# Kernel optimization log

Hardware: AMD Instinct MI355X
Metric: run time of the kernel (lower is better)

Reference implementation:

```python
import jax, jax.numpy as jnp
import numpy as np
from jax import lax

WINDOW = 3  # box-filter window (matches init kwarg)


def setup_inputs() -> dict:
    key = jax.random.key(0)
    y_pred = jax.random.normal(key, (1, 3, 192, 192, 192), dtype=jnp.float32)
    return {"y_pred": y_pred}


def _box_filter(x, win):
    pad = win // 2
    kernel = jnp.ones((3, 1, win, win, win), dtype=x.dtype) / (win ** 3)
    return lax.conv_general_dilated(
        x, kernel,
        window_strides=(1, 1, 1),
        padding=[(pad, pad)] * 3,
        dimension_numbers=("NCDHW", "OIDHW", "NCDHW"),
        feature_group_count=3,
    )


def reference(y_pred):
    base = y_pred[:, :, :-1, :-1, :-1]
    dy = jnp.abs(y_pred[:, :, 1:, :-1, :-1] - base)
    dx = jnp.abs(y_pred[:, :, :-1, 1:, :-1] - base)
    dz = jnp.abs(y_pred[:, :, :-1, :-1, 1:] - base)

    fdx = _box_filter(dx, WINDOW)  # [B,3,D-1,H-1,W-1]
    fdy = _box_filter(dy, WINDOW)
    fdz = _box_filter(dz, WINDOW)

    dxdx, dxdy, dxdz = fdx[:, 1:2], fdy[:, 1:2], fdz[:, 1:2]
    dydx, dydy, dydz = fdx[:, 0:1], fdy[:, 0:1], fdz[:, 0:1]
    dzdx, dzdy, dzdz = fdx[:, 2:3], fdy[:, 2:3], fdz[:, 2:3]

    det_1 = (dxdx + 1) * ((dydy + 1) * (dzdz + 1) - dydz * dzdy)
    det_2 = -dxdy * (dydx * (dzdz + 1) - dydz * dzdx)
    det_3 = dxdz * (dydx * dzdy - (dydy + 1) * dzdx)
    J = det_1 + det_2 + det_3
    return jnp.squeeze(J)  # [D-1, H-1, W-1] for B=1
```

## Files before the change

kernel.cpp:

```cpp
#include <hip/hip_runtime.h>

#define NSZ   192
#define NSZ2  (NSZ*NSZ)
#define NSZ3  (NSZ*NSZ*NSZ)
#define N1    191
#define TW    64
#define TH    8
#define TD    8
#define LROWS 11
#define PADW  72
#define ROWF4 18
#define NROWS 33
#define SLOTF4 (NROWS*ROWF4)
#define SLOTF  (SLOTF4*4)
#define NTHREADS 256

__device__ __forceinline__ void ld3f2(float* d, const float* p) {
    *(float2*)&d[0] = *(const float2*)&p[0];
    *(float2*)&d[2] = *(const float2*)&p[2];
    *(float2*)&d[4] = *(const float2*)&p[4];
}

__global__ __launch_bounds__(NTHREADS)
void jac_kernel(const float* __restrict__ y, float* __restrict__ out) {
    __shared__ __align__(16) float lds[3 * SLOTF];

    const int tx = threadIdx.x;
    const int ty = threadIdx.y;
    const int tid = ty * 32 + tx;
    const int w0 = blockIdx.x * TW;
    const int h0 = blockIdx.y * TH;
    const int d0 = blockIdx.z * TD;
    const int j  = h0 + ty;
    const int k0 = w0 + 2 * tx;

    float mrow[3][4];
    #pragma unroll
    for (int r = 0; r < 3; ++r) {
        int gr = j - 1 + r;
        float rv = (gr >= 0 && gr < N1) ? 1.f : 0.f;
        #pragma unroll
        for (int p = 0; p < 4; ++p) {
            int gk = k0 - 1 + p;
            mrow[r][p] = (gk >= 0 && gk < N1) ? rv : 0.f;
        }
    }

    const bool has3 = (tid < SLOTF4 - 2 * NTHREADS);
    int goff[3];
    #pragma unroll
    for (int k = 0; k < 3; ++k) {
        int e4 = tid + k * NTHREADS;
        int e4c = e4 < SLOTF4 ? e4 : 0;
        int rowidx = e4c / ROWF4;
        int m   = e4c - rowidx * ROWF4;
        int ch  = rowidx / LROWS;
        int row = rowidx - ch * LROWS;
        int gr = h0 - 1 + row; gr = gr < 0 ? 0 : (gr > N1 ? N1 : gr);
        int c4 = w0 - 4 + 4 * m; c4 = c4 < 0 ? 0 : (c4 > NSZ - 4 ? NSZ - 4 : c4);
        goff[k] = ch * NSZ3 + gr * NSZ + c4;
    }

    float PS[18], T1[18];
    #pragma unroll
    for (int t = 0; t < 18; ++t) { PS[t] = 0.f; T1[t] = 0.f; }

    {
        float4 s0a, s0b, s0c, s1a, s1b, s1c;
        const bool p0 = (d0 >= 1);
        if (p0) {
            const float* b = y + (size_t)(d0 - 1) * NSZ2;
            s0a = *(const float4*)&b[goff[0]];
            s0b = *(const float4*)&b[goff[1]];
            if (has3) s0c = *(const float4*)&b[goff[2]];
        }
        {
            const float* b = y + (size_t)d0 * NSZ2;
            s1a = *(const float4*)&b[goff[0]];
            s1b = *(const float4*)&b[goff[1]];
            if (has3) s1c = *(const float4*)&b[goff[2]];
        }
        if (p0) {
            float* d = lds + ((d0 + 2) % 3) * SLOTF;
            *(float4*)&d[tid * 4] = s0a;
            *(float4*)&d[(tid + 256) * 4] = s0b;
            if (has3) *(float4*)&d[(tid + 512) * 4] = s0c;
        }
        {
            float* d = lds + (d0 % 3) * SLOTF;
            *(float4*)&d[tid * 4] = s1a;
            *(float4*)&d[(tid + 256) * 4] = s1b;
            if (has3) *(float4*)&d[(tid + 512) * 4] = s1c;
        }
    }
    __syncthreads();

    int sA = (d0 + 2) % 3;

    for (int ii = 0; ii < TD + 2; ++ii) {
        const int i  = d0 - 1 + ii;
        const int sB = sA == 2 ? 0 : sA + 1;
        const int sC = sB == 2 ? 0 : sB + 1;

        const bool doStage = (ii <= TD) && (i + 2 <= N1);
        float4 g0, g1, g2;
        if (doStage) {
            const float* b = y + (size_t)(i + 2) * NSZ2;
            g0 = *(const float4*)&b[goff[0]];
            g1 = *(const float4*)&b[goff[1]];
            if (has3) g2 = *(const float4*)&b[goff[2]];
        }

        float acc[18];
        #pragma unroll
        for (int t = 0; t < 18; ++t) acc[t] = 0.f;

        if (i >= 0 && i < N1) {
            #pragma unroll
            for (int c = 0; c < 3; ++c) {
                const float* pA = lds + sA * SLOTF + (c * LROWS + ty) * PADW + 2 * tx + 2;
                const float* pB = lds + sB * SLOTF + (c * LROWS + ty) * PADW + 2 * tx + 2;
                float Y0[6], Y1[6], Z0[6];
                ld3f2(Y0, pA);
                #pragma unroll
                for (int r = 0; r < 3; ++r) {
                    ld3f2(Y1, pA + (r + 1) * PADW);
                    ld3f2(Z0, pB + r * PADW);
                    float dxv[4], dyv[4], dzv[4];
                    #pragma unroll
                    for (int p = 0; p < 4; ++p) {
                        float m = mrow[r][p];
                        dxv[p] = fabsf(Y1[p + 1] - Y0[p + 1]) * m;
                        dyv[p] = fabsf(Z0[p + 1] - Y0[p + 1]) * m;
                        dzv[p] = fabsf(Y0[p + 2] - Y0[p + 1]) * m;
                    }
                    #pragma unroll
                    for (int q = 0; q < 2; ++q) {
                        acc[(c * 3 + 0) * 2 + q] += dxv[q] + dxv[q + 1] + dxv[q + 2];
                        acc[(c * 3 + 1) * 2 + q] += dyv[q] + dyv[q + 1] + dyv[q + 2];
                        acc[(c * 3 + 2) * 2 + q] += dzv[q] + dzv[q + 1] + dzv[q + 2];
                    }
                    #pragma unroll
                    for (int p = 0; p < 6; ++p) Y0[p] = Y1[p];
                }
            }
        }

        float f[18];
        #pragma unroll
        for (int t = 0; t < 18; ++t) {
            f[t]  = PS[t] + acc[t];
            PS[t] = T1[t] + acc[t];
            T1[t] = acc[t];
        }

        const int d = i - 1;
        if (ii >= 2 && d < N1 && j < N1) {
            const float s27 = 1.f / 27.f;
            #pragma unroll
            for (int q = 0; q < 2; ++q) {
                if (k0 + q < N1) {
                    float axx = f[(1*3+0)*2+q]*s27, axy = f[(1*3+1)*2+q]*s27, axz = f[(1*3+2)*2+q]*s27;
                    float ayx = f[(0*3+0)*2+q]*s27, ayy = f[(0*3+1)*2+q]*s27, ayz = f[(0*3+2)*2+q]*s27;
                    float azx = f[(2*3+0)*2+q]*s27, azy = f[(2*3+1)*2+q]*s27, azz = f[(2*3+2)*2+q]*s27;
                    float ee = ayy + 1.f, zz = azz + 1.f;
                    float J = (axx + 1.f) * (ee*zz - ayz*azy)
                            - axy * (ayx*zz - ayz*azx)
                            + axz * (ayx*azy - ee*azx);
                    out[(d * N1 + j) * N1 + (k0 + q)] = J;
                }
            }
        }

        if (doStage) {
            float* dst = lds + sC * SLOTF;
            *(float4*)&dst[tid * 4] = g0;
            *(float4*)&dst[(tid + 256) * 4] = g1;
            if (has3) *(float4*)&dst[(tid + 512) * 4] = g2;
        }
        __syncthreads();

        sA = sB;
    }
}

extern "C" void kernel_launch(void* const* d_in, const int* in_sizes, int n_in,
                              void* d_out, int out_size, void* d_ws, size_t ws_size,
                              hipStream_t stream) {
    const float* y = (const float*)d_in[0];
    float* out = (float*)d_out;
    dim3 grid(3, 24, 24);
    dim3 block(32, 8, 1);
    jac_kernel<<<grid, block, 0, stream>>>(y, out);
}
```

Baseline: 62.03 us.

## Stage input slices via direct global-to-LDS loads with taller tiles and 4 outputs/thread

Replaces register-staged global loads with __builtin_amdgcn_global_load_lds so slices go straight into LDS. The tile height doubles to 16, which cuts halo overhead, and each thread now computes 4 W-outputs instead of 2. The masking is split into separate column and row factors, and the 1/27 scaling is folded into a single final multiply. The goal is less register traffic and halo reload, at the cost of more registers (36-entry accumulators) and fewer blocks. The async LDS loads are ordered only by the existing __syncthreads, which relies on the compiler inserting a waitcnt.

```diff
diff --git a/kernel.cpp b/kernel.cpp
--- a/kernel.cpp
+++ b/kernel.cpp
@@ -5,55 +5,73 @@
 #define NSZ3  (NSZ*NSZ*NSZ)
 #define N1    191
 #define TW    64
-#define TH    8
+#define TH    16
 #define TD    8
-#define LROWS 11
+#define LROWS 19
 #define PADW  72
 #define ROWF4 18
-#define NROWS 33
-#define SLOTF4 (NROWS*ROWF4)
-#define SLOTF  (SLOTF4*4)
+#define SLOTF4R 1026
+#define SLOTF4P 1088
+#define SLOTF  (SLOTF4P*4)
 #define NTHREADS 256
 
-__device__ __forceinline__ void ld3f2(float* d, const float* p) {
+__device__ __forceinline__ void gload_lds16(const float* g, float* l) {
+    __builtin_amdgcn_global_load_lds((const __attribute__((address_space(1))) void*)g,
+                                     (__attribute__((address_space(3))) void*)l, 16, 0, 0);
+}
+
+__device__ __forceinline__ void ld8(float* d, const float* p) {
     *(float2*)&d[0] = *(const float2*)&p[0];
     *(float2*)&d[2] = *(const float2*)&p[2];
     *(float2*)&d[4] = *(const float2*)&p[4];
-}
-
-__global__ __launch_bounds__(NTHREADS)
+    *(float2*)&d[6] = *(const float2*)&p[6];
+}
+
+__device__ __forceinline__ void stage(const float* __restrict__ y, float* slot,
+                                      int s, const int* goff, int tid) {
+    const float* src = y + (size_t)s * NSZ2;
+    gload_lds16(src + goff[0], slot + (size_t)tid * 4);
+    gload_lds16(src + goff[1], slot + (size_t)(tid + 256) * 4);
+    gload_lds16(src + goff[2], slot + (size_t)(tid + 512) * 4);
+    gload_lds16(src + goff[3], slot + (size_t)(tid + 768) * 4);
+    if (tid < 64)
+        gload_lds16(src + goff[4], slot + (size_t)(1024 + tid) * 4);
+}
+
+#define IDX(c,dir,q) (((c)*3+(dir))*4+(q))
+
+__global__ __launch_bounds__(NTHREADS, 3)
 void jac_kernel(const float* __restrict__ y, float* __restrict__ out) {
     __shared__ __align__(16) float lds[3 * SLOTF];
 
     const int tx = threadIdx.x;
     const int ty = threadIdx.y;
-    const int tid = ty * 32 + tx;
+    const int tid = ty * 16 + tx;
     const int w0 = blockIdx.x * TW;
     const int h0 = blockIdx.y * TH;
     const int d0 = blockIdx.z * TD;
     const int j  = h0 + ty;
-    const int k0 = w0 + 2 * tx;
-
-    float mrow[3][4];
+    const int k0 = w0 + 4 * tx;
+
+    float colv[6], rowv[3];
+    #pragma unroll
+    for (int p = 0; p < 6; ++p) {
+        int gk = k0 - 1 + p;
+        colv[p] = (gk >= 0 && gk < N1) ? 1.f : 0.f;
+    }
     #pragma unroll
     for (int r = 0; r < 3; ++r) {
         int gr = j - 1 + r;
-        float rv = (gr >= 0 && gr < N1) ? 1.f : 0.f;
-        #pragma unroll
-        for (int p = 0; p < 4; ++p) {
-            int gk = k0 - 1 + p;
-            mrow[r][p] = (gk >= 0 && gk < N1) ? rv : 0.f;
-        }
-    }
-
-    const bool has3 = (tid < SLOTF4 - 2 * NTHREADS);
-    int goff[3];
-    #pragma unroll
-    for (int k = 0; k < 3; ++k) {
-        int e4 = tid + k * NTHREADS;
-        int e4c = e4 < SLOTF4 ? e4 : 0;
-        int rowidx = e4c / ROWF4;
-        int m   = e4c - rowidx * ROWF4;
+        rowv[r] = (gr >= 0 && gr < N1) ? 1.f : 0.f;
+    }
+
+    int goff[5];
+    #pragma unroll
+    for (int k = 0; k < 5; ++k) {
+        int e4 = (k < 4) ? (tid + k * 256) : (1024 + (tid & 63));
+        if (e4 > SLOTF4R - 1) e4 = SLOTF4R - 1;
+        int rowidx = e4 / ROWF4;
+        int m   = e4 - rowidx * ROWF4;
         int ch  = rowidx / LROWS;
         int row = rowidx - ch * LROWS;
         int gr = h0 - 1 + row; gr = gr < 0 ? 0 : (gr > N1 ? N1 : gr);
@@ -61,125 +79,114 @@
         goff[k] = ch * NSZ3 + gr * NSZ + c4;
     }
 
-    float PS[18], T1[18];
-    #pragma unroll
-    for (int t = 0; t < 18; ++t) { PS[t] = 0.f; T1[t] = 0.f; }
-
-    {
-        float4 s0a, s0b, s0c, s1a, s1b, s1c;
-        const bool p0 = (d0 >= 1);
-        if (p0) {
-            const float* b = y + (size_t)(d0 - 1) * NSZ2;
-            s0a = *(const float4*)&b[goff[0]];
-            s0b = *(const float4*)&b[goff[1]];
-            if (has3) s0c = *(const float4*)&b[goff[2]];
-        }
-        {
-            const float* b = y + (size_t)d0 * NSZ2;
-            s1a = *(const float4*)&b[goff[0]];
-            s1b = *(const float4*)&b[goff[1]];
-            if (has3) s1c = *(const float4*)&b[goff[2]];
-        }
-        if (p0) {
-            float* d = lds + ((d0 + 2) % 3) * SLOTF;
-            *(float4*)&d[tid * 4] = s0a;
-            *(float4*)&d[(tid + 256) * 4] = s0b;
-            if (has3) *(float4*)&d[(tid + 512) * 4] = s0c;
-        }
-        {
-            float* d = lds + (d0 % 3) * SLOTF;
-            *(float4*)&d[tid * 4] = s1a;
-            *(float4*)&d[(tid + 256) * 4] = s1b;
-            if (has3) *(float4*)&d[(tid + 512) * 4] = s1c;
-        }
-    }
+    float a1[36], a2[36];
+    #pragma unroll
+    for (int t = 0; t < 36; ++t) { a1[t] = 0.f; a2[t] = 0.f; }
+
+    if (d0 >= 1) stage(y, lds + ((d0 + 2) % 3) * SLOTF, d0 - 1, goff, tid);
+    stage(y, lds + (d0 % 3) * SLOTF, d0, goff, tid);
     __syncthreads();
 
     int sA = (d0 + 2) % 3;
+    const int wbase = 4 * tx + 2;
 
     for (int ii = 0; ii < TD + 2; ++ii) {
         const int i  = d0 - 1 + ii;
         const int sB = sA == 2 ? 0 : sA + 1;
         const int sC = sB == 2 ? 0 : sB + 1;
 
-        const bool doStage = (ii <= TD) && (i + 2 <= N1);
-        float4 g0, g1, g2;
-        if (doStage) {
-            const float* b = y + (size_t)(i + 2) * NSZ2;
-            g0 = *(const float4*)&b[goff[0]];
-            g1 = *(const float4*)&b[goff[1]];
-            if (has3) g2 = *(const float4*)&b[goff[2]];
-        }
-
-        float acc[18];
-        #pragma unroll
-        for (int t = 0; t < 18; ++t) acc[t] = 0.f;
+        if (ii <= TD && i + 2 <= N1)
+            stage(y, lds + sC * SLOTF, i + 2, goff, tid);
+
+        float f[36];
 
         if (i >= 0 && i < N1) {
             #pragma unroll
             for (int c = 0; c < 3; ++c) {
-                const float* pA = lds + sA * SLOTF + (c * LROWS + ty) * PADW + 2 * tx + 2;
-                const float* pB = lds + sB * SLOTF + (c * LROWS + ty) * PADW + 2 * tx + 2;
-                float Y0[6], Y1[6], Z0[6];
-                ld3f2(Y0, pA);
+                const float* pA = lds + sA * SLOTF + (c * LROWS + ty) * PADW + wbase;
+                const float* pB = lds + sB * SLOTF + (c * LROWS + ty) * PADW + wbase;
+                float acc[12];
+                float Y0[8], Y1[8], Z0[8];
+                ld8(Y0, pA);
                 #pragma unroll
                 for (int r = 0; r < 3; ++r) {
-                    ld3f2(Y1, pA + (r + 1) * PADW);
-                    ld3f2(Z0, pB + r * PADW);
-                    float dxv[4], dyv[4], dzv[4];
+                    ld8(Y1, pA + (r + 1) * PADW);
+                    ld8(Z0, pB + r * PADW);
+                    const float rv = rowv[r];
+                    float dH[6], dD[6], dW[6];
                     #pragma unroll
-                    for (int p = 0; p < 4; ++p) {
-                        float m = mrow[r][p];
-                        dxv[p] = fabsf(Y1[p + 1] - Y0[p + 1]) * m;
-                        dyv[p] = fabsf(Z0[p + 1] - Y0[p + 1]) * m;
-                        dzv[p] = fabsf(Y0[p + 2] - Y0[p + 1]) * m;
+                    for (int p = 0; p < 6; ++p) {
+                        const float cm = colv[p];
+                        dH[p] = fabsf(Y1[p + 1] - Y0[p + 1]) * cm;
+                        dD[p] = fabsf(Z0[p + 1] - Y0[p + 1]) * cm;
+                        dW[p] = fabsf(Y0[p + 2] - Y0[p + 1]) * cm;
+                    }
+                    {
+                        float e12 = dH[1] + dH[2], e34 = dH[3] + dH[4];
+                        float t0 = dH[0] + e12, t1 = e12 + dH[3];
+                        float t2 = dH[2] + e34, t3 = e34 + dH[5];
+                        if (r == 0) { acc[0] = rv * t0; acc[1] = rv * t1; acc[2] = rv * t2; acc[3] = rv * t3; }
+                        else { acc[0] = fmaf(rv, t0, acc[0]); acc[1] = fmaf(rv, t1, acc[1]);
+                               acc[2] = fmaf(rv, t2, acc[2]); acc[3] = fmaf(rv, t3, acc[3]); }
+                    }
+                    {
+                        float e12 = dD[1] + dD[2], e34 = dD[3] + dD[4];
+                        float t0 = dD[0] + e12, t1 = e12 + dD[3];
+                        float t2 = dD[2] + e34, t3 = e34 + dD[5];
+                        if (r == 0) { acc[4] = rv * t0; acc[5] = rv * t1; acc[6] = rv * t2; acc[7] = rv * t3; }
+                        else { acc[4] = fmaf(rv, t0, acc[4]); acc[5] = fmaf(rv, t1, acc[5]);
+                               acc[6] = fmaf(rv, t2, acc[6]); acc[7] = fmaf(rv, t3, acc[7]); }
+                    }
+                    {
+                        float e12 = dW[1] + dW[2], e34 = dW[3] + dW[4];
+                        float t0 = dW[0] + e12, t1 = e12 + dW[3];
+                        float t2 = dW[2] + e34, t3 = e34 + dW[5];
+                        if (r == 0) { acc[8] = rv * t0; acc[9] = rv * t1; acc[10] = rv * t2; acc[11] = rv * t3; }
+                        else { acc[8] = fmaf(rv, t0, acc[8]); acc[9] = fmaf(rv, t1, acc[9]);
+                               acc[10] = fmaf(rv, t2, acc[10]); acc[11] = fmaf(rv, t3, acc[11]); }
                     }
                     #pragma unroll
-                    for (int q = 0; q < 2; ++q) {
-                        acc[(c * 3 + 0) * 2 + q] += dxv[q] + dxv[q + 1] + dxv[q + 2];
-                        acc[(c * 3 + 1) * 2 + q] += dyv[q] + dyv[q + 1] + dyv[q + 2];
-                        acc[(c * 3 + 2) * 2 + q] += dzv[q] + dzv[q + 1] + dzv[q + 2];
-                    }
-                    #pragma unroll
-                    for (int p = 0; p < 6; ++p) Y0[p] = Y1[p];
+                    for (int p = 0; p < 8; ++p) Y0[p] = Y1[p];
+                }
+                #pragma unroll
+                for (int t = 0; t < 12; ++t) {
+                    const int gi = c * 12 + t;
+                    f[gi]  = a2[gi] + a1[gi] + acc[t];
+                    a2[gi] = a1[gi];
+                    a1[gi] = acc[t];
+                }
+            }
+        } else {
+            #pragma unroll
+            for (int t = 0; t < 36; ++t) {
+                f[t]  = a2[t] + a1[t];
+                a2[t] = a1[t];
+                a1[t] = 0.f;
+            }
+        }
+
+        const int d = i - 1;
+        if (ii >= 2 && d < N1 && j < N1) {
+            const float K = 27.f, KS = 1.f / 19683.f;
+            #pragma unroll
+            for (int q = 0; q < 4; ++q) {
+                if (k0 + q < N1) {
+                    float ayx = f[IDX(0,0,q)], ayy = f[IDX(0,1,q)], ayz = f[IDX(0,2,q)];
+                    float axx = f[IDX(1,0,q)], axy = f[IDX(1,1,q)], axz = f[IDX(1,2,q)];
+                    float azx = f[IDX(2,0,q)], azy = f[IDX(2,1,q)], azz = f[IDX(2,2,q)];
+                    float ayy27 = ayy + K, azz27 = azz + K, axx27 = axx + K;
+                    float t = fmaf(-ayz, azy, ayy27 * azz27);
+                    float v = fmaf(-ayz, azx, ayx * azz27);
+                    float w = fmaf(-ayy27, azx, ayx * azy);
+                    float R = axx27 * t;
+                    R = fmaf(-axy, v, R);
+                    R = fmaf(axz, w, R);
+                    out[(d * N1 + j) * N1 + (k0 + q)] = R * KS;
                 }
             }
         }
 
-        float f[18];
-        #pragma unroll
-        for (int t = 0; t < 18; ++t) {
-            f[t]  = PS[t] + acc[t];
-            PS[t] = T1[t] + acc[t];
-            T1[t] = acc[t];
-        }
-
-        const int d = i - 1;
-        if (ii >= 2 && d < N1 && j < N1) {
-            const float s27 = 1.f / 27.f;
-            #pragma unroll
-            for (int q = 0; q < 2; ++q) {
-                if (k0 + q < N1) {
-                    float axx = f[(1*3+0)*2+q]*s27, axy = f[(1*3+1)*2+q]*s27, axz = f[(1*3+2)*2+q]*s27;
-                    float ayx = f[(0*3+0)*2+q]*s27, ayy = f[(0*3+1)*2+q]*s27, ayz = f[(0*3+2)*2+q]*s27;
-                    float azx = f[(2*3+0)*2+q]*s27, azy = f[(2*3+1)*2+q]*s27, azz = f[(2*3+2)*2+q]*s27;
-                    float ee = ayy + 1.f, zz = azz + 1.f;
-                    float J = (axx + 1.f) * (ee*zz - ayz*azy)
-                            - axy * (ayx*zz - ayz*azx)
-                            + axz * (ayx*azy - ee*azx);
-                    out[(d * N1 + j) * N1 + (k0 + q)] = J;
-                }
-            }
-        }
-
-        if (doStage) {
-            float* dst = lds + sC * SLOTF;
-            *(float4*)&dst[tid * 4] = g0;
-            *(float4*)&dst[(tid + 256) * 4] = g1;
-            if (has3) *(float4*)&dst[(tid + 512) * 4] = g2;
-        }
         __syncthreads();
-
         sA = sB;
     }
 }
@@ -189,7 +196,7 @@
                               hipStream_t stream) {
     const float* y = (const float*)d_in[0];
     float* out = (float*)d_out;
-    dim3 grid(3, 24, 24);
-    dim3 block(32, 8, 1);
+    dim3 grid(3, 12, 24);
+    dim3 block(16, 16, 1);
     jac_kernel<<<grid, block, 0, stream>>>(y, out);
 }
```

Result: slower. 149.0 us (+140.2%).
